# Kernel tuning notes

Measured on AMD Instinct MI355X. Metric: run time of the kernel, lower is better.

Reference implementation:

```python
import jax, jax.numpy as jnp
import numpy as np

H = 128
N = 20000
E = 640000

def _lin_params(key, fan_in, fan_out, bias=True):
    k1, k2 = jax.random.split(key)
    bound = 1.0 / np.sqrt(fan_in)
    W = jax.random.uniform(k1, (fan_in, fan_out), jnp.float32, -bound, bound)
    if bias:
        b = jax.random.uniform(k2, (fan_out,), jnp.float32, -bound, bound)
        return W, b
    return W, None

def setup_inputs() -> dict:
    key = jax.random.key(0)
    ks = jax.random.split(key, 10)
    h = jax.random.normal(ks[0], (N, H), jnp.float32)
    pos = jax.random.normal(ks[1], (N, 3), jnp.float32)
    edge_index = jax.random.randint(ks[2], (2, E), 0, N, jnp.int64)
    eW1, eb1 = _lin_params(ks[3], 2 * H + 1, H)
    eW2, eb2 = _lin_params(ks[4], H, H)
    cW1, cb1 = _lin_params(ks[5], H, H)
    cW2, _ = _lin_params(ks[6], H, 1, bias=False)
    nW1, nb1 = _lin_params(ks[7], 2 * H, H)
    nW2, nb2 = _lin_params(ks[8], H, H)
    return {"h": h, "pos": pos, "edge_index": edge_index,
            "eW1": eW1, "eb1": eb1, "eW2": eW2, "eb2": eb2,
            "cW1": cW1, "cb1": cb1, "cW2": cW2,
            "nW1": nW1, "nb1": nb1, "nW2": nW2, "nb2": nb2}

def reference(h, pos, edge_index, eW1, eb1, eW2, eb2, cW1, cb1, cW2, nW1, nb1, nW2, nb2):
    row, col = edge_index[0], edge_index[1]
    n = h.shape[0]
    # per-edge geometry
    coord_diff = pos[row] - pos[col]                      # [E, 3]
    sq_dists = jnp.sum(coord_diff ** 2, axis=-1, keepdims=True)  # [E, 1]
    # edge MLP: Linear -> SiLU -> Linear -> SiLU
    edge_inputs = jnp.concatenate([h[row], h[col], sq_dists], axis=-1)  # [E, 2H+1]
    m_ij = jax.nn.silu(jax.nn.silu(edge_inputs @ eW1 + eb1) @ eW2 + eb2)  # [E, H]
    # coord MLP: Linear -> SiLU -> Linear(no bias) -> scalar weight per edge
    coord_weights = jax.nn.silu(m_ij @ cW1 + cb1) @ cW2   # [E, 1]
    norm_coord_diff = coord_diff / jnp.sqrt(sq_dists + 1e-8)
    pos_updates_ij = norm_coord_diff * coord_weights      # [E, 3]
    # scatter-mean over target nodes (zero where a node has no edges)
    pos_sum = jax.ops.segment_sum(pos_updates_ij, row, num_segments=n)
    cnt = jax.ops.segment_sum(jnp.ones((row.shape[0], 1), h.dtype), row, num_segments=n)
    pos_out = pos + pos_sum / jnp.maximum(cnt, 1.0)
    # scatter-add messages, then node MLP with residual
    m_i = jax.ops.segment_sum(m_ij, row, num_segments=n)  # [N, H]
    node_inputs = jnp.concatenate([h, m_i], axis=-1)      # [N, 2H]
    h_out = h + (jax.nn.silu(node_inputs @ nW1 + nb1) @ nW2 + nb2)
    return h_out, pos_out
```

## Files before the change

kernel.cpp:

```cpp
#include <hip/hip_runtime.h>
#include <hip/hip_bf16.h>
#include <cstdint>

#define H 128
#define NNODES 20000
#define NEDGES 640000
#define TILE 64
#define PQ_BLOCKS 313

typedef unsigned short ushort_t;
typedef __attribute__((ext_vector_type(8))) short short8;
typedef __attribute__((ext_vector_type(4))) float floatx4;
typedef __attribute__((ext_vector_type(2))) float floatx2;

__device__ __forceinline__ ushort_t f2bf(float f){
  uint32_t u = __builtin_bit_cast(uint32_t, f);
  u += 0x7fffu + ((u >> 16) & 1u);
  return (ushort_t)(u >> 16);
}
__device__ __forceinline__ uint32_t pk2bf(float lo, float hi){
  __hip_bfloat162 h2 = __float22bfloat162_rn(make_float2(lo, hi));
  uint32_t u;
  __builtin_memcpy(&u, &h2, 4);
  return u;
}
__device__ __forceinline__ floatx2 bfpair2(uint32_t u){
  floatx2 r;
  r.x = __builtin_bit_cast(float, u << 16);
  r.y = __builtin_bit_cast(float, u & 0xffff0000u);
  return r;
}
__device__ __forceinline__ float silu_f(float x){
  float e = __builtin_amdgcn_exp2f(-1.44269504089f * x);
  return x * __builtin_amdgcn_rcpf(1.f + e);
}

__global__ void setup_kernel(const float* __restrict__ eW1, const float* __restrict__ eW2,
                             const float* __restrict__ cW1, const float* __restrict__ nW1,
                             const float* __restrict__ nW2, const int* __restrict__ ei,
                             ushort_t* __restrict__ eW1t, ushort_t* __restrict__ eW2t,
                             ushort_t* __restrict__ cW1t, ushort_t* __restrict__ nW1t,
                             ushort_t* __restrict__ nW2t, uint32_t* __restrict__ w256b,
                             int* __restrict__ hist, float4* __restrict__ zbase){
  int idx = blockIdx.x * 256 + threadIdx.x;
  if (idx < 32768){
    int n = idx >> 8, k = idx & 255;
    eW1t[idx] = f2bf(eW1[k * H + n]);
  } else if (idx < 49152){
    int j = idx - 32768; int n = j >> 7, k = j & 127;
    eW2t[j] = f2bf(eW2[k * H + n]);
  } else if (idx < 65536){
    int j = idx - 49152; int n = j >> 7, k = j & 127;
    cW1t[j] = f2bf(cW1[k * H + n]);
  } else if (idx < 98304){
    int j = idx - 65536; int n = j >> 8, k = j & 255;
    nW1t[j] = f2bf(nW1[k * H + n]);
  } else if (idx < 114688){
    int j = idx - 98304; int n = j >> 7, k = j & 127;
    nW2t[j] = f2bf(nW2[k * H + n]);
  } else if (idx < 114752){
    int j = idx - 114688;
    w256b[j] = pk2bf(eW1[256 * H + 2*j], eW1[256 * H + 2*j + 1]);
  } else if (idx < 754752){
    int j = idx - 114752;
    atomicAdd(&hist[ei[j]], 1);
  } else {
    int j = idx - 754752;
    if (j < 655000) zbase[j] = make_float4(0.f, 0.f, 0.f, 0.f);
  }
}

__global__ void scan_kernel(const int* __restrict__ hist, int* __restrict__ head){
  __shared__ int s[1024];
  const int t = threadIdx.x;
  const int base = t * 20;
  int loc[20];
  int sum = 0;
  #pragma unroll
  for (int i = 0; i < 20; i++){
    int idx = base + i;
    int v = (idx < NNODES) ? hist[idx] : 0;
    loc[i] = sum;
    sum += v;
  }
  s[t] = sum;
  __syncthreads();
  for (int off = 1; off < 1024; off <<= 1){
    int tmp = (t >= off) ? s[t - off] : 0;
    __syncthreads();
    s[t] += tmp;
    __syncthreads();
  }
  int offv = s[t] - sum;
  #pragma unroll
  for (int i = 0; i < 20; i++){
    int idx = base + i;
    if (idx < NNODES) head[idx] = offv + loc[i];
  }
}

__global__ void pqscatter_kernel(const float* __restrict__ h,
                                 const ushort_t* __restrict__ eW1t,
                                 const ushort_t* __restrict__ nW1t,
                                 const float* __restrict__ eb1,
                                 ushort_t* __restrict__ Pb, ushort_t* __restrict__ Qb,
                                 ushort_t* __restrict__ Rb,
                                 const int* __restrict__ ei, int* __restrict__ head,
                                 int2* __restrict__ spair){
  if (blockIdx.x >= PQ_BLOCKS){
    int idx = (blockIdx.x - PQ_BLOCKS) * 256 + threadIdx.x;
    if (idx < NEDGES){
      int r = ei[idx], c = ei[NEDGES + idx];
      int p = atomicAdd(&head[r], 1);
      spair[p] = make_int2(r, c);
    }
    return;
  }
  const int t = threadIdx.x;
  const int lane = t & 63, q = lane >> 4, ln = lane & 15;
  const int nb = (t >> 6) * 32;
  const int c0 = nb + 2 * ln;
  const int base = blockIdx.x * 64;

  floatx4 accP[4][2], accQ[4][2], accR[4][2];
  #pragma unroll
  for (int mt = 0; mt < 4; mt++)
    #pragma unroll
    for (int nt = 0; nt < 2; nt++){
      accP[mt][nt] = (floatx4)0.f; accQ[mt][nt] = (floatx4)0.f; accR[mt][nt] = (floatx4)0.f;
    }

  #pragma unroll
  for (int ks = 0; ks < 4; ks++){
    short8 a[4];
    #pragma unroll
    for (int mt = 0; mt < 4; mt++){
      int node = base + mt*16 + ln;
      if (node >= NNODES) node = NNODES - 1;
      const float* hp = h + (size_t)node * H + ks*32 + q*8;
      float4 v0 = *(const float4*)hp;
      float4 v1 = *(const float4*)(hp + 4);
      uint32_t tw[4];
      tw[0] = pk2bf(v0.x, v0.y); tw[1] = pk2bf(v0.z, v0.w);
      tw[2] = pk2bf(v1.x, v1.y); tw[3] = pk2bf(v1.z, v1.w);
      __builtin_memcpy(&a[mt], tw, 16);
    }
    short8 bP[2], bQ[2], bR[2];
    #pragma unroll
    for (int nt = 0; nt < 2; nt++){
      bP[nt] = *(const short8*)(eW1t + (size_t)(c0 + nt) * 256 + ks*32 + q*8);
      bQ[nt] = *(const short8*)(eW1t + (size_t)(c0 + nt) * 256 + 128 + ks*32 + q*8);
      bR[nt] = *(const short8*)(nW1t + (size_t)(c0 + nt) * 256 + ks*32 + q*8);
    }
    #pragma unroll
    for (int mt = 0; mt < 4; mt++)
      #pragma unroll
      for (int nt = 0; nt < 2; nt++){
        accP[mt][nt] = __builtin_amdgcn_mfma_f32_16x16x32_bf16(a[mt], bP[nt], accP[mt][nt], 0, 0, 0);
        accQ[mt][nt] = __builtin_amdgcn_mfma_f32_16x16x32_bf16(a[mt], bQ[nt], accQ[mt][nt], 0, 0, 0);
        accR[mt][nt] = __builtin_amdgcn_mfma_f32_16x16x32_bf16(a[mt], bR[nt], accR[mt][nt], 0, 0, 0);
      }
  }
  float2 e1 = *(const float2*)(eb1 + c0);
  #pragma unroll
  for (int mt = 0; mt < 4; mt++)
    #pragma unroll
    for (int r = 0; r < 4; r++){
      int node = base + mt*16 + q*4 + r;
      if (node < NNODES){
        *(uint32_t*)(Pb + (size_t)node * H + c0) = pk2bf(accP[mt][0][r] + e1.x, accP[mt][1][r] + e1.y);
        *(uint32_t*)(Qb + (size_t)node * H + c0) = pk2bf(accQ[mt][0][r], accQ[mt][1][r]);
        *(uint32_t*)(Rb + (size_t)node * H + c0) = pk2bf(accR[mt][0][r], accR[mt][1][r]);
      }
    }
}

__global__ __launch_bounds__(256, 8) void edge_kernel(
    const ushort_t* __restrict__ Pb, const ushort_t* __restrict__ Qb,
    const float* __restrict__ pos, const int2* __restrict__ spair,
    const uint32_t* __restrict__ w256b,
    const float* __restrict__ eb2, const float* __restrict__ cb1,
    const float* __restrict__ cW2,
    const ushort_t* __restrict__ eW2t, const ushort_t* __restrict__ cW1t,
    float* __restrict__ m_i, float* __restrict__ pos_sum)
{
  __shared__ __align__(16) ushort_t buf[TILE * 136];
  __shared__ int   row_l[TILE];
  __shared__ float sq_l[TILE];
  __shared__ float dx_l[TILE], dy_l[TILE], dz_l[TILE];
  __shared__ float wbuf[TILE][4];

  const int t = threadIdx.x;
  const int base = blockIdx.x * TILE;
  const int w = t >> 6;
  const int lane = t & 63, q = lane >> 4, ln = lane & 15;
  const int nb = w * 32;
  const int c0 = nb + 2 * ln;

  {
    const int i = t >> 2, p = t & 3;
    int2 rc = spair[base + i];
    float ax = pos[rc.x*3+0] - pos[rc.y*3+0];
    float ay = pos[rc.x*3+1] - pos[rc.y*3+1];
    float az = pos[rc.x*3+2] - pos[rc.y*3+2];
    float sq = ax*ax + ay*ay + az*az;
    if (p == 0){
      row_l[i] = rc.x; sq_l[i] = sq;
      dx_l[i] = ax; dy_l[i] = ay; dz_l[i] = az;
    }
    floatx2 sq2; sq2.x = sq; sq2.y = sq;
    const uint4* Pp = (const uint4*)(Pb + (size_t)rc.x * H + p*32);
    const uint4* Qp = (const uint4*)(Qb + (size_t)rc.y * H + p*32);
    const uint4* Wp = (const uint4*)(w256b + p*16);
    ushort_t* dst = buf + i * 136 + p*32;
    #pragma unroll
    for (int j = 0; j < 4; j++){
      uint4 pv = Pp[j], qv = Qp[j], wv = Wp[j];
      uint32_t pvv[4] = {pv.x, pv.y, pv.z, pv.w};
      uint32_t qvv[4] = {qv.x, qv.y, qv.z, qv.w};
      uint32_t wvv[4] = {wv.x, wv.y, wv.z, wv.w};
      uint32_t outv[4];
      #pragma unroll
      for (int e = 0; e < 4; e++){
        floatx2 f = bfpair2(pvv[e]) + bfpair2(qvv[e]) + sq2 * bfpair2(wvv[e]);
        outv[e] = pk2bf(silu_f(f.x), silu_f(f.y));
      }
      uint4 out; __builtin_memcpy(&out, outv, 16);
      *(uint4*)(dst + j*8) = out;
    }
  }
  __syncthreads();

  floatx4 acc[4][2];

  #pragma unroll
  for (int mt = 0; mt < 4; mt++)
    #pragma unroll
    for (int nt = 0; nt < 2; nt++) acc[mt][nt] = (floatx4)0.f;
  #pragma unroll
  for (int ks = 0; ks < 4; ks++){
    short8 a[4], b[2];
    #pragma unroll
    for (int mt = 0; mt < 4; mt++)
      a[mt] = *(const short8*)(buf + (mt*16 + ln) * 136 + ks*32 + q*8);
    #pragma unroll
    for (int nt = 0; nt < 2; nt++)
      b[nt] = *(const short8*)(eW2t + (size_t)(c0 + nt) * 128 + ks*32 + q*8);
    #pragma unroll
    for (int mt = 0; mt < 4; mt++)
      #pragma unroll
      for (int nt = 0; nt < 2; nt++)
        acc[mt][nt] = __builtin_amdgcn_mfma_f32_16x16x32_bf16(a[mt], b[nt], acc[mt][nt], 0, 0, 0);
  }
  __syncthreads();
  {
    float2 e2 = *(const float2*)(eb2 + c0);
    #pragma unroll
    for (int mt = 0; mt < 4; mt++)
      #pragma unroll
      for (int r = 0; r < 4; r++){
        int m = mt*16 + q*4 + r;
        float f0 = silu_f(acc[mt][0][r] + e2.x);
        float f1 = silu_f(acc[mt][1][r] + e2.y);
        *(uint32_t*)(buf + m * 136 + c0) = pk2bf(f0, f1);
      }
  }
  __syncthreads();

  #pragma unroll
  for (int mt = 0; mt < 4; mt++)
    #pragma unroll
    for (int nt = 0; nt < 2; nt++) acc[mt][nt] = (floatx4)0.f;
  #pragma unroll
  for (int ks = 0; ks < 4; ks++){
    short8 a[4], b[2];
    #pragma unroll
    for (int mt = 0; mt < 4; mt++)
      a[mt] = *(const short8*)(buf + (mt*16 + ln) * 136 + ks*32 + q*8);
    #pragma unroll
    for (int nt = 0; nt < 2; nt++)
      b[nt] = *(const short8*)(cW1t + (size_t)(c0 + nt) * 128 + ks*32 + q*8);
    #pragma unroll
    for (int mt = 0; mt < 4; mt++)
      #pragma unroll
      for (int nt = 0; nt < 2; nt++)
        acc[mt][nt] = __builtin_amdgcn_mfma_f32_16x16x32_bf16(a[mt], b[nt], acc[mt][nt], 0, 0, 0);
  }
  {
    float2 c1 = *(const float2*)(cb1 + c0);
    float2 c2 = *(const float2*)(cW2 + c0);
    #pragma unroll
    for (int mt = 0; mt < 4; mt++)
      #pragma unroll
      for (int r = 0; r < 4; r++){
        float p = silu_f(acc[mt][0][r] + c1.x) * c2.x
                + silu_f(acc[mt][1][r] + c1.y) * c2.y;
        p += __shfl_xor(p, 1);
        p += __shfl_xor(p, 2);
        p += __shfl_xor(p, 4);
        p += __shfl_xor(p, 8);
        if (ln == 0) wbuf[mt*16 + q*4 + r][w] = p;
      }
  }
  __syncthreads();

  if (t < 128){
    int cp = (t & 63) * 2;
    int ms = (t >> 6) * 32;
    float a0 = 0.f, a1 = 0.f;
    int cur = row_l[ms];
    #pragma unroll 4
    for (int mm = 0; mm < 32; mm++){
      int m = ms + mm;
      int rr = row_l[m];
      uint32_t v = *(const uint32_t*)(buf + m * 136 + cp);
      if (rr != cur){
        unsafeAtomicAdd(&m_i[(size_t)cur * H + cp],     a0);
        unsafeAtomicAdd(&m_i[(size_t)cur * H + cp + 1], a1);
        a0 = 0.f; a1 = 0.f; cur = rr;
      }
      floatx2 f = bfpair2(v);
      a0 += f.x; a1 += f.y;
    }
    unsafeAtomicAdd(&m_i[(size_t)cur * H + cp],     a0);
    unsafeAtomicAdd(&m_i[(size_t)cur * H + cp + 1], a1);
  } else if (t < 131){
    const int d = t - 128;
    const float* src = (d == 0) ? dx_l : (d == 1) ? dy_l : dz_l;
    float accv = 0.f;
    int cur = row_l[0];
    for (int m = 0; m < TILE; m++){
      int rr = row_l[m];
      if (rr != cur){
        unsafeAtomicAdd(&pos_sum[cur*3 + d], accv);
        accv = 0.f; cur = rr;
      }
      float wv = wbuf[m][0] + wbuf[m][1] + wbuf[m][2] + wbuf[m][3];
      float s = __builtin_amdgcn_rsqf(sq_l[m] + 1e-8f) * wv;
      accv += src[m] * s;
    }
    unsafeAtomicAdd(&pos_sum[cur*3 + d], accv);
  }
}

__global__ __launch_bounds__(256, 8) void node_kernel(
    const float* __restrict__ h, const float* __restrict__ pos,
    const float* __restrict__ nb1, const float* __restrict__ nb2,
    const ushort_t* __restrict__ nW1t, const ushort_t* __restrict__ nW2t,
    const ushort_t* __restrict__ Rb,
    const float* __restrict__ m_i, const float* __restrict__ pos_sum,
    const int* __restrict__ hist,
    float* __restrict__ h_out, float* __restrict__ pos_out)
{
  __shared__ __align__(16) ushort_t bufT[32 * 136];
  const int t = threadIdx.x;
  const int base = blockIdx.x * 32;
  const int lane = t & 63, q = lane >> 4, ln = lane & 15;
  const int nb_ = (t >> 6) * 32;
  const int c0 = nb_ + 2 * ln;

  if (t < 32){
    int node = base + t;
    float c = fmaxf((float)hist[node], 1.f);
    float invc = __builtin_amdgcn_rcpf(c);
    pos_out[node*3+0] = pos[node*3+0] + pos_sum[node*3+0] * invc;
    pos_out[node*3+1] = pos[node*3+1] + pos_sum[node*3+1] * invc;
    pos_out[node*3+2] = pos[node*3+2] + pos_sum[node*3+2] * invc;
  }

  floatx4 acc[2][2];
  #pragma unroll
  for (int mt = 0; mt < 2; mt++)
    #pragma unroll
    for (int nt = 0; nt < 2; nt++) acc[mt][nt] = (floatx4)0.f;
  #pragma unroll
  for (int ks = 0; ks < 4; ks++){
    short8 a[2], b[2];
    #pragma unroll
    for (int mt = 0; mt < 2; mt++){
      const float* mp = m_i + (size_t)(base + mt*16 + ln) * H + ks*32 + q*8;
      float4 v0 = *(const float4*)mp;
      float4 v1 = *(const float4*)(mp + 4);
      uint32_t tw[4];
      tw[0] = pk2bf(v0.x, v0.y); tw[1] = pk2bf(v0.z, v0.w);
      tw[2] = pk2bf(v1.x, v1.y); tw[3] = pk2bf(v1.z, v1.w);
      __builtin_memcpy(&a[mt], tw, 16);
    }
    #pragma unroll
    for (int nt = 0; nt < 2; nt++)
      b[nt] = *(const short8*)(nW1t + (size_t)(c0 + nt) * 256 + 128 + ks*32 + q*8);
    #pragma unroll
    for (int mt = 0; mt < 2; mt++)
      #pragma unroll
      for (int nt = 0; nt < 2; nt++)
        acc[mt][nt] = __builtin_amdgcn_mfma_f32_16x16x32_bf16(a[mt], b[nt], acc[mt][nt], 0, 0, 0);
  }
  {
    float2 b1 = *(const float2*)(nb1 + c0);
    #pragma unroll
    for (int mt = 0; mt < 2; mt++)
      #pragma unroll
      for (int r = 0; r < 4; r++){
        int m = mt*16 + q*4 + r;
        int node = base + m;
        floatx2 rf = bfpair2(*(const uint32_t*)(Rb + (size_t)node * H + c0));
        float f0 = silu_f(acc[mt][0][r] + rf.x + b1.x);
        float f1 = silu_f(acc[mt][1][r] + rf.y + b1.y);
        *(uint32_t*)(bufT + m * 136 + c0) = pk2bf(f0, f1);
      }
  }
  __syncthreads();

  #pragma unroll
  for (int mt = 0; mt < 2; mt++)
    #pragma unroll
    for (int nt = 0; nt < 2; nt++) acc[mt][nt] = (floatx4)0.f;
  #pragma unroll
  for (int ks = 0; ks < 4; ks++){
    short8 a[2], b[2];
    #pragma unroll
    for (int mt = 0; mt < 2; mt++)
      a[mt] = *(const short8*)(bufT + (mt*16 + ln) * 136 + ks*32 + q*8);
    #pragma unroll
    for (int nt = 0; nt < 2; nt++)
      b[nt] = *(const short8*)(nW2t + (size_t)(c0 + nt) * 128 + ks*32 + q*8);
    #pragma unroll
    for (int mt = 0; mt < 2; mt++)
      #pragma unroll
      for (int nt = 0; nt < 2; nt++)
        acc[mt][nt] = __builtin_amdgcn_mfma_f32_16x16x32_bf16(a[mt], b[nt], acc[mt][nt], 0, 0, 0);
  }
  {
    float2 b2 = *(const float2*)(nb2 + c0);
    #pragma unroll
    for (int mt = 0; mt < 2; mt++)
      #pragma unroll
      for (int r = 0; r < 4; r++){
        int node = base + mt*16 + q*4 + r;
        const float2 hv = *(const float2*)(h + (size_t)node * H + c0);
        float2 o;
        o.x = hv.x + acc[mt][0][r] + b2.x;
        o.y = hv.y + acc[mt][1][r] + b2.y;
        *(float2*)(h_out + (size_t)node * H + c0) = o;
      }
  }
}

extern "C" void kernel_launch(void* const* d_in, const int* in_sizes, int n_in,
                              void* d_out, int out_size, void* d_ws, size_t ws_size,
                              hipStream_t stream){
  const float* h   = (const float*)d_in[0];
  const float* pos = (const float*)d_in[1];
  const int*   ei  = (const int*)d_in[2];
  const float* eW1 = (const float*)d_in[3];
  const float* eb1 = (const float*)d_in[4];
  const float* eW2 = (const float*)d_in[5];
  const float* eb2 = (const float*)d_in[6];
  const float* cW1 = (const float*)d_in[7];
  const float* cb1 = (const float*)d_in[8];
  const float* cW2 = (const float*)d_in[9];
  const float* nW1 = (const float*)d_in[10];
  const float* nb1 = (const float*)d_in[11];
  const float* nW2 = (const float*)d_in[12];
  const float* nb2 = (const float*)d_in[13];

  char* ws = (char*)d_ws;
  float*    m_i     = (float*)   (ws);
  float*    pos_sum = (float*)   (ws + 10240000);
  int*      hist    = (int*)     (ws + 10480000);
  int*      head    = (int*)     (ws + 10560000);
  int2*     spair   = (int2*)    (ws + 10644096);
  ushort_t* Pb      = (ushort_t*)(ws + 15764096);
  ushort_t* eW1t    = (ushort_t*)(ws + 20884096);
  ushort_t* eW2t    = (ushort_t*)(ws + 20949632);
  ushort_t* cW1t    = (ushort_t*)(ws + 20982400);
  ushort_t* nW1t    = (ushort_t*)(ws + 21015168);
  ushort_t* nW2t    = (ushort_t*)(ws + 21080704);
  ushort_t* Qb      = (ushort_t*)(ws + 21113472);
  ushort_t* Rb      = (ushort_t*)(ws + 26233472);
  uint32_t* w256b   = (uint32_t*)(ws + 31353472);

  (void)hipMemsetAsync(hist, 0, 80000, stream);

  setup_kernel<<<5507, 256, 0, stream>>>(eW1, eW2, cW1, nW1, nW2, ei,
                                         eW1t, eW2t, cW1t, nW1t, nW2t, w256b, hist,
                                         (float4*)ws);
  scan_kernel<<<1, 1024, 0, stream>>>(hist, head);
  pqscatter_kernel<<<PQ_BLOCKS + (NEDGES + 255) / 256, 256, 0, stream>>>(
      h, eW1t, nW1t, eb1, Pb, Qb, Rb, ei, head, spair);

  edge_kernel<<<NEDGES / TILE, 256, 0, stream>>>(Pb, Qb, pos, spair, w256b,
                                                 eb2, cb1, cW2,
                                                 eW2t, cW1t, m_i, pos_sum);

  float* h_out   = (float*)d_out;
  float* pos_out = h_out + (size_t)NNODES * H;
  node_kernel<<<NNODES / 32, 256, 0, stream>>>(h, pos, nb1, nb2,
                                               nW1t, nW2t, Rb, m_i, pos_sum,
                                               hist, h_out, pos_out);
}
```

Baseline: 358.7 us.

## Fuse node MLP into edge kernel via ticket counter and grid-wide wait

The separate node kernel is merged into the tail of the edge kernel. Each block takes a ticket from an atomic counter after its edge work. The last 625 tickets spin until every edge block has checked in, then run the node MLP and position update for one 32-node tile each, reusing the edge kernel's shared buffer. This removes one kernel launch and its gap. In exchange it adds a spin-wait that relies on waiting blocks not starving unscheduled ones, and fence-based visibility of the atomics to m_i and pos_sum.

New measurement: 1.406 ms. 3.92x slower.

```diff
diff --git a/kernel.cpp b/kernel.cpp
--- a/kernel.cpp
+++ b/kernel.cpp
@@ -7,6 +7,8 @@
 #define NEDGES 640000
 #define TILE 64
 #define PQ_BLOCKS 313
+#define EDGE_BLOCKS (NEDGES / TILE)
+#define NODE_TILES 625
 
 typedef unsigned short ushort_t;
 typedef __attribute__((ext_vector_type(8))) short short8;
@@ -182,13 +184,19 @@
     const float* __restrict__ eb2, const float* __restrict__ cb1,
     const float* __restrict__ cW2,
     const ushort_t* __restrict__ eW2t, const ushort_t* __restrict__ cW1t,
-    float* __restrict__ m_i, float* __restrict__ pos_sum)
+    float* __restrict__ m_i, float* __restrict__ pos_sum,
+    const float* __restrict__ h, const float* __restrict__ nb1,
+    const float* __restrict__ nb2, const ushort_t* __restrict__ nW1t,
+    const ushort_t* __restrict__ nW2t, const ushort_t* __restrict__ Rb,
+    const int* __restrict__ hist, int* __restrict__ cnt,
+    float* __restrict__ h_out, float* __restrict__ pos_out)
 {
   __shared__ __align__(16) ushort_t buf[TILE * 136];
   __shared__ int   row_l[TILE];
   __shared__ float sq_l[TILE];
   __shared__ float dx_l[TILE], dy_l[TILE], dz_l[TILE];
   __shared__ float wbuf[TILE][4];
+  __shared__ int   ticket_s;
 
   const int t = threadIdx.x;
   const int base = blockIdx.x * TILE;
@@ -341,26 +349,24 @@
     }
     unsafeAtomicAdd(&pos_sum[cur*3 + d], accv);
   }
-}
-
-__global__ __launch_bounds__(256, 8) void node_kernel(
-    const float* __restrict__ h, const float* __restrict__ pos,
-    const float* __restrict__ nb1, const float* __restrict__ nb2,
-    const ushort_t* __restrict__ nW1t, const ushort_t* __restrict__ nW2t,
-    const ushort_t* __restrict__ Rb,
-    const float* __restrict__ m_i, const float* __restrict__ pos_sum,
-    const int* __restrict__ hist,
-    float* __restrict__ h_out, float* __restrict__ pos_out)
-{
-  __shared__ __align__(16) ushort_t bufT[32 * 136];
-  const int t = threadIdx.x;
-  const int base = blockIdx.x * 32;
-  const int lane = t & 63, q = lane >> 4, ln = lane & 15;
-  const int nb_ = (t >> 6) * 32;
-  const int c0 = nb_ + 2 * ln;
+
+  __threadfence();
+  __syncthreads();
+  if (t == 0) ticket_s = atomicAdd(cnt, 1);
+  __syncthreads();
+  const int ticket = ticket_s;
+  if (ticket < EDGE_BLOCKS - NODE_TILES) return;
+
+  if (t == 0){
+    while (atomicAdd(cnt, 0) < EDGE_BLOCKS) __builtin_amdgcn_s_sleep(8);
+  }
+  __syncthreads();
+  __threadfence();
+
+  const int nbase = (ticket - (EDGE_BLOCKS - NODE_TILES)) * 32;
 
   if (t < 32){
-    int node = base + t;
+    int node = nbase + t;
     float c = fmaxf((float)hist[node], 1.f);
     float invc = __builtin_amdgcn_rcpf(c);
     pos_out[node*3+0] = pos[node*3+0] + pos_sum[node*3+0] * invc;
@@ -368,17 +374,17 @@
     pos_out[node*3+2] = pos[node*3+2] + pos_sum[node*3+2] * invc;
   }
 
-  floatx4 acc[2][2];
+  floatx4 nacc[2][2];
   #pragma unroll
   for (int mt = 0; mt < 2; mt++)
     #pragma unroll
-    for (int nt = 0; nt < 2; nt++) acc[mt][nt] = (floatx4)0.f;
+    for (int nt = 0; nt < 2; nt++) nacc[mt][nt] = (floatx4)0.f;
   #pragma unroll
   for (int ks = 0; ks < 4; ks++){
     short8 a[2], b[2];
     #pragma unroll
     for (int mt = 0; mt < 2; mt++){
-      const float* mp = m_i + (size_t)(base + mt*16 + ln) * H + ks*32 + q*8;
+      const float* mp = m_i + (size_t)(nbase + mt*16 + ln) * H + ks*32 + q*8;
       float4 v0 = *(const float4*)mp;
       float4 v1 = *(const float4*)(mp + 4);
       uint32_t tw[4];
@@ -393,7 +399,7 @@
     for (int mt = 0; mt < 2; mt++)
       #pragma unroll
       for (int nt = 0; nt < 2; nt++)
-        acc[mt][nt] = __builtin_amdgcn_mfma_f32_16x16x32_bf16(a[mt], b[nt], acc[mt][nt], 0, 0, 0);
+        nacc[mt][nt] = __builtin_amdgcn_mfma_f32_16x16x32_bf16(a[mt], b[nt], nacc[mt][nt], 0, 0, 0);
   }
   {
     float2 b1 = *(const float2*)(nb1 + c0);
@@ -402,11 +408,11 @@
       #pragma unroll
       for (int r = 0; r < 4; r++){
         int m = mt*16 + q*4 + r;
-        int node = base + m;
+        int node = nbase + m;
         floatx2 rf = bfpair2(*(const uint32_t*)(Rb + (size_t)node * H + c0));
-        float f0 = silu_f(acc[mt][0][r] + rf.x + b1.x);
-        float f1 = silu_f(acc[mt][1][r] + rf.y + b1.y);
-        *(uint32_t*)(bufT + m * 136 + c0) = pk2bf(f0, f1);
+        float f0 = silu_f(nacc[mt][0][r] + rf.x + b1.x);
+        float f1 = silu_f(nacc[mt][1][r] + rf.y + b1.y);
+        *(uint32_t*)(buf + m * 136 + c0) = pk2bf(f0, f1);
       }
   }
   __syncthreads();
@@ -414,13 +420,13 @@
   #pragma unroll
   for (int mt = 0; mt < 2; mt++)
     #pragma unroll
-    for (int nt = 0; nt < 2; nt++) acc[mt][nt] = (floatx4)0.f;
+    for (int nt = 0; nt < 2; nt++) nacc[mt][nt] = (floatx4)0.f;
   #pragma unroll
   for (int ks = 0; ks < 4; ks++){
     short8 a[2], b[2];
     #pragma unroll
     for (int mt = 0; mt < 2; mt++)
-      a[mt] = *(const short8*)(bufT + (mt*16 + ln) * 136 + ks*32 + q*8);
+      a[mt] = *(const short8*)(buf + (mt*16 + ln) * 136 + ks*32 + q*8);
     #pragma unroll
     for (int nt = 0; nt < 2; nt++)
       b[nt] = *(const short8*)(nW2t + (size_t)(c0 + nt) * 128 + ks*32 + q*8);
@@ -428,7 +434,7 @@
     for (int mt = 0; mt < 2; mt++)
       #pragma unroll
       for (int nt = 0; nt < 2; nt++)
-        acc[mt][nt] = __builtin_amdgcn_mfma_f32_16x16x32_bf16(a[mt], b[nt], acc[mt][nt], 0, 0, 0);
+        nacc[mt][nt] = __builtin_amdgcn_mfma_f32_16x16x32_bf16(a[mt], b[nt], nacc[mt][nt], 0, 0, 0);
   }
   {
     float2 b2 = *(const float2*)(nb2 + c0);
@@ -436,11 +442,11 @@
     for (int mt = 0; mt < 2; mt++)
       #pragma unroll
       for (int r = 0; r < 4; r++){
-        int node = base + mt*16 + q*4 + r;
+        int node = nbase + mt*16 + q*4 + r;
         const float2 hv = *(const float2*)(h + (size_t)node * H + c0);
         float2 o;
-        o.x = hv.x + acc[mt][0][r] + b2.x;
-        o.y = hv.y + acc[mt][1][r] + b2.y;
+        o.x = hv.x + nacc[mt][0][r] + b2.x;
+        o.y = hv.y + nacc[mt][1][r] + b2.y;
         *(float2*)(h_out + (size_t)node * H + c0) = o;
       }
   }
@@ -468,7 +474,8 @@
   float*    m_i     = (float*)   (ws);
   float*    pos_sum = (float*)   (ws + 10240000);
   int*      hist    = (int*)     (ws + 10480000);
-  int*      head    = (int*)     (ws + 10560000);
+  int*      cnt     = (int*)     (ws + 10560000);
+  int*      head    = (int*)     (ws + 10560256);
   int2*     spair   = (int2*)    (ws + 10644096);
   ushort_t* Pb      = (ushort_t*)(ws + 15764096);
   ushort_t* eW1t    = (ushort_t*)(ws + 20884096);
@@ -480,7 +487,7 @@
   ushort_t* Rb      = (ushort_t*)(ws + 26233472);
   uint32_t* w256b   = (uint32_t*)(ws + 31353472);
 
-  (void)hipMemsetAsync(hist, 0, 80000, stream);
+  (void)hipMemsetAsync(hist, 0, 80004, stream);
 
   setup_kernel<<<5507, 256, 0, stream>>>(eW1, eW2, cW1, nW1, nW2, ei,
                                          eW1t, eW2t, cW1t, nW1t, nW2t, w256b, hist,
@@ -489,13 +496,11 @@
   pqscatter_kernel<<<PQ_BLOCKS + (NEDGES + 255) / 256, 256, 0, stream>>>(
       h, eW1t, nW1t, eb1, Pb, Qb, Rb, ei, head, spair);
 
-  edge_kernel<<<NEDGES / TILE, 256, 0, stream>>>(Pb, Qb, pos, spair, w256b,
-                                                 eb2, cb1, cW2,
-                                                 eW2t, cW1t, m_i, pos_sum);
-
   float* h_out   = (float*)d_out;
   float* pos_out = h_out + (size_t)NNODES * H;
-  node_kernel<<<NNODES / 32, 256, 0, stream>>>(h, pos, nb1, nb2,
-                                               nW1t, nW2t, Rb, m_i, pos_sum,
-                                               hist, h_out, pos_out);
-}
+  edge_kernel<<<EDGE_BLOCKS, 256, 0, stream>>>(Pb, Qb, pos, spair, w256b,
+                                               eb2, cb1, cW2, eW2t, cW1t,
+                                               m_i, pos_sum,
+                                               h, nb1, nb2, nW1t, nW2t, Rb,
+                                               hist, cnt, h_out, pos_out);
+}
```
